# Kernel tuning notes

Hardware: AMD Instinct MI355X
Metric: run time of the kernel (lower is better)

## Reference

```python
import jax, jax.numpy as jnp
import numpy as np

B, T, C, H = 2, 2048, 512, 8
HD = C // H  # head size = 64

def _layernorm(x, g, b, eps=1e-5):
    mu = jnp.mean(x, axis=-1, keepdims=True)
    var = jnp.var(x, axis=-1, keepdims=True)
    return (x - mu) * jax.lax.rsqrt(var + eps) * g + b

def setup_inputs() -> dict:
    key = jax.random.key(0)
    ks = jax.random.split(key, 12)
    s_attn = 1.0 / np.sqrt(C)
    s_proj = 1.0 / np.sqrt(H * HD)
    s_ffn1 = 1.0 / np.sqrt(C)
    s_ffn2 = 1.0 / np.sqrt(4 * C)
    return {
        "x":   jax.random.normal(ks[0], (B, T, C), jnp.float32),
        "Wq":  jax.random.uniform(ks[1], (H, C, HD), jnp.float32, -s_attn, s_attn),
        "Wk":  jax.random.uniform(ks[2], (H, C, HD), jnp.float32, -s_attn, s_attn),
        "Wv":  jax.random.uniform(ks[3], (H, C, HD), jnp.float32, -s_attn, s_attn),
        "Wo":  jax.random.uniform(ks[4], (H * HD, C), jnp.float32, -s_proj, s_proj),
        "bo":  jax.random.uniform(ks[5], (C,), jnp.float32, -s_proj, s_proj),
        "W1":  jax.random.uniform(ks[6], (C, 4 * C), jnp.float32, -s_ffn1, s_ffn1),
        "b1":  jax.random.uniform(ks[7], (4 * C,), jnp.float32, -s_ffn1, s_ffn1),
        "W2":  jax.random.uniform(ks[8], (4 * C, C), jnp.float32, -s_ffn2, s_ffn2),
        "b2":  jax.random.uniform(ks[9], (C,), jnp.float32, -s_ffn2, s_ffn2),
        "g1":  jnp.ones((C,), jnp.float32),
        "be1": jnp.zeros((C,), jnp.float32),
        "g2":  jnp.ones((C,), jnp.float32),
        "be2": jnp.zeros((C,), jnp.float32),
    }

def reference(x, Wq, Wk, Wv, Wo, bo, W1, b1, W2, b2, g1, be1, g2, be2):
    # --- multi-head causal self-attention on ln1(x) ---
    h = _layernorm(x, g1, be1)
    q = jnp.einsum("btc,hcd->bhtd", h, Wq)
    k = jnp.einsum("btc,hcd->bhtd", h, Wk)
    v = jnp.einsum("btc,hcd->bhtd", h, Wv)
    scores = jnp.einsum("bhtd,bhsd->bhts", q, k) * (HD ** -0.5)
    causal = jnp.tril(jnp.ones((T, T), bool))
    scores = jnp.where(causal, scores, -jnp.inf)
    wei = jax.nn.softmax(scores, axis=-1)
    attn = jnp.einsum("bhts,bhsd->bhtd", wei, v)
    attn = attn.transpose(0, 2, 1, 3).reshape(B, T, H * HD)  # concat heads
    x = x + attn @ Wo + bo
    # --- GELU MLP on ln2(x) ---
    h2 = _layernorm(x, g2, be2)
    ff = jax.nn.gelu(h2 @ W1 + b1, approximate=False) @ W2 + b2
    return x + ff
```

## Files before the change

kernel.cpp:

```cpp
#include <hip/hip_runtime.h>
#include <math.h>

constexpr int B_   = 2;
constexpr int T_   = 2048;
constexpr int C_   = 512;
constexpr int H_   = 8;
constexpr int HD_  = 64;
constexpr int M_   = B_ * T_;
constexpr int FF_  = 4 * C_;
constexpr int NQKV_ = 3 * C_;

typedef __attribute__((ext_vector_type(8))) short short8;
typedef __attribute__((ext_vector_type(4))) short short4v;
typedef __attribute__((ext_vector_type(4))) float floatx4;

static __device__ __forceinline__ unsigned short f2bf(float f) {
    union { float f; unsigned u; } v; v.f = f;
    unsigned r = v.u + 0x7fff + ((v.u >> 16) & 1);
    return (unsigned short)(r >> 16);
}

static __device__ __forceinline__ unsigned packbf2(float a, float b) {
    union { float f; unsigned u; } x, y; x.f = a; y.f = b;
    unsigned lo = (x.u + 0x7fff + ((x.u >> 16) & 1)) >> 16;
    unsigned hi = (y.u + 0x7fff + ((y.u >> 16) & 1)) & 0xffff0000u;
    return lo | hi;
}

static __device__ __forceinline__ void gl2lds16(const unsigned short* g,
                                                unsigned short* l) {
    __builtin_amdgcn_global_load_lds(
        (const __attribute__((address_space(1))) void*)g,
        (__attribute__((address_space(3))) void*)l, 16, 0, 0);
}

#if __has_builtin(__builtin_amdgcn_mfma_f32_16x16x16bf16_1k)
static __device__ __forceinline__ floatx4 mfma16(short4v a, short4v b, floatx4 c) {
    return __builtin_amdgcn_mfma_f32_16x16x16bf16_1k(a, b, c, 0, 0, 0);
}
#elif __has_builtin(__builtin_amdgcn_mfma_f32_16x16x16_bf16)
static __device__ __forceinline__ floatx4 mfma16(short4v a, short4v b, floatx4 c) {
    return __builtin_amdgcn_mfma_f32_16x16x16_bf16(a, b, c, 0, 0, 0);
}
#else
static __device__ __forceinline__ floatx4 mfma16(short4v a, short4v b, floatx4 c) {
    asm volatile("v_mfma_f32_16x16x16_bf16 %0, %1, %2, %0"
                 : "+v"(c) : "v"(a), "v"(b));
    return c;
}
#endif

__global__ void prep_weights(const float* __restrict__ Wq,
                             const float* __restrict__ Wk,
                             const float* __restrict__ Wv,
                             const float* __restrict__ Wo,
                             const float* __restrict__ W1,
                             const float* __restrict__ W2,
                             unsigned short* __restrict__ Wqkv_t,
                             unsigned short* __restrict__ Wo_t,
                             unsigned short* __restrict__ W1_t,
                             unsigned short* __restrict__ W2_t) {
    __shared__ float tile[32][33];
    int idx = blockIdx.x;
    const float* src; unsigned short* dst;
    int K, N, k0, n0;
    float scale = 1.0f;
    if (idx < 768) {
        int wz = idx >> 8, rem = idx & 255;
        int h = rem >> 5, r2 = rem & 31;
        k0 = (r2 >> 1) * 32; n0 = (r2 & 1) * 32;
        src = (wz == 0 ? Wq : (wz == 1 ? Wk : Wv)) + (size_t)h * C_ * HD_;
        dst = Wqkv_t + (size_t)(wz * C_ + h * HD_) * C_;
        K = C_; N = HD_;
        if (wz == 0) scale = 0.125f;
    } else if (idx < 1024) {
        int rem = idx - 768;
        n0 = (rem & 15) * 32; k0 = (rem >> 4) * 32;
        src = Wo; dst = Wo_t; K = C_; N = C_;
    } else if (idx < 2048) {
        int rem = idx - 1024;
        n0 = (rem & 63) * 32; k0 = (rem >> 6) * 32;
        src = W1; dst = W1_t; K = C_; N = FF_;
    } else {
        int rem = idx - 2048;
        n0 = (rem & 15) * 32; k0 = (rem >> 4) * 32;
        src = W2; dst = W2_t; K = FF_; N = C_;
    }
    int tx = threadIdx.x, ty = threadIdx.y;
#pragma unroll
    for (int i = 0; i < 4; i++)
        tile[ty + i * 8][tx] = src[(size_t)(k0 + ty + i * 8) * N + n0 + tx];
    __syncthreads();
#pragma unroll
    for (int i = 0; i < 4; i++)
        dst[(size_t)(n0 + ty + i * 8) * K + k0 + tx] = f2bf(tile[tx][ty + i * 8] * scale);
}

__global__ void v_transpose(const unsigned short* __restrict__ qkv,
                            unsigned short* __restrict__ vT) {
    __shared__ unsigned short tile[32][33];
    int bh = blockIdx.z, b = bh >> 3, h = bh & 7;
    int t0 = blockIdx.x * 32, d0 = blockIdx.y * 32;
    int tx = threadIdx.x, ty = threadIdx.y;
#pragma unroll
    for (int i = 0; i < 4; i++)
        tile[ty + i * 8][tx] = qkv[(size_t)(b * T_ + t0 + ty + i * 8) * NQKV_
                                   + 2 * C_ + h * HD_ + d0 + tx];
    __syncthreads();
#pragma unroll
    for (int i = 0; i < 4; i++)
        vT[(size_t)(bh * HD_ + d0 + ty + i * 8) * T_ + t0 + tx] = tile[tx][ty + i * 8];
}

__global__ void ln_kernel(const float* __restrict__ x,
                          const float* __restrict__ g,
                          const float* __restrict__ b,
                          unsigned short* __restrict__ out) {
    int row  = blockIdx.x;
    int lane = threadIdx.x;
    const float* xr = x + (size_t)row * C_;
    int c0 = lane * 8;
    float4 v0 = *(const float4*)(xr + c0);
    float4 v1 = *(const float4*)(xr + c0 + 4);
    float vals[8] = {v0.x, v0.y, v0.z, v0.w, v1.x, v1.y, v1.z, v1.w};

    float s = 0.f, ss = 0.f;
#pragma unroll
    for (int j = 0; j < 8; j++) { s += vals[j]; ss += vals[j] * vals[j]; }
#pragma unroll
    for (int off = 32; off; off >>= 1) {
        s  += __shfl_xor(s,  off);
        ss += __shfl_xor(ss, off);
    }
    float mu  = s / C_;
    float var = ss / C_ - mu * mu;
    float rs  = rsqrtf(var + 1e-5f);

    unsigned short* orow = out + (size_t)row * C_;
#pragma unroll
    for (int j = 0; j < 8; j++) {
        int c = c0 + j;
        orow[c] = f2bf((vals[j] - mu) * rs * g[c] + b[c]);
    }
}

template<int BM, int BN, int BK>
__global__ __launch_bounds__(256) void mfma_gemm(
        const unsigned short* __restrict__ A,
        const unsigned short* __restrict__ Bt,
        const float* __restrict__ bias,
        const float* __restrict__ resid,
        float* __restrict__ outF,
        unsigned short* __restrict__ outB,
        int M, int N, int K, int flags) {
    constexpr int WM = BM / 2, WN = BN / 2;
    constexpr int MI = WM / 16, NI = WN / 16, KH = BK / 32;
    __shared__ unsigned short As[KH * BM * 32];
    __shared__ unsigned short Bs[KH * BN * 32];

    int t = threadIdx.x;
    int lane = t & 63, w = t >> 6;
    int wr = (w >> 1) * WM, wc = (w & 1) * WN;
    int lm = lane & 15, lq = lane >> 4;
    int m0 = blockIdx.y * BM, n0 = blockIdx.x * BN;

    floatx4 acc[MI][NI];
#pragma unroll
    for (int mi = 0; mi < MI; mi++)
#pragma unroll
        for (int ni = 0; ni < NI; ni++) acc[mi][ni] = (floatx4){0.f, 0.f, 0.f, 0.f};

    for (int k0 = 0; k0 < K; k0 += BK) {
        __syncthreads();
#pragma unroll
        for (int hh = 0; hh < KH; hh++) {
#pragma unroll
            for (int j = 0; j < BM * 4 / 256; j++) {
                int i = t + j * 256;
                gl2lds16(A + (size_t)(m0 + (i >> 2)) * K + k0 + hh * 32 + (i & 3) * 8,
                         &As[hh * BM * 32 + i * 8]);
            }
#pragma unroll
            for (int j = 0; j < BN * 4 / 256; j++) {
                int i = t + j * 256;
                gl2lds16(Bt + (size_t)(n0 + (i >> 2)) * K + k0 + hh * 32 + (i & 3) * 8,
                         &Bs[hh * BN * 32 + i * 8]);
            }
        }
        __syncthreads();

#pragma unroll
        for (int hh = 0; hh < KH; hh++) {
            short8 af[MI], bfv[NI];
#pragma unroll
            for (int mi = 0; mi < MI; mi++)
                af[mi] = *(const short8*)&As[hh * BM * 32 + (wr + mi * 16 + lm) * 32 + lq * 8];
#pragma unroll
            for (int ni = 0; ni < NI; ni++)
                bfv[ni] = *(const short8*)&Bs[hh * BN * 32 + (wc + ni * 16 + lm) * 32 + lq * 8];
#pragma unroll
            for (int mi = 0; mi < MI; mi++)
#pragma unroll
                for (int ni = 0; ni < NI; ni++)
                    acc[mi][ni] = __builtin_amdgcn_mfma_f32_16x16x32_bf16(
                        af[mi], bfv[ni], acc[mi][ni], 0, 0, 0);
        }
    }

#pragma unroll
    for (int mi = 0; mi < MI; mi++)
#pragma unroll
        for (int ni = 0; ni < NI; ni++) {
            int gc = n0 + wc + ni * 16 + lm;
#pragma unroll
            for (int r = 0; r < 4; r++) {
                int gr = m0 + wr + mi * 16 + lq * 4 + r;
                float v = acc[mi][ni][r];
                if (flags & 1) v += bias[gc];
                if (flags & 4) v = 0.5f * v * (1.0f + erff(v * 0.70710678118654752f));
                if (flags & 2) v += resid[(size_t)gr * N + gc];
                if (flags & 8) outB[(size_t)gr * N + gc] = f2bf(v);
                else           outF[(size_t)gr * N + gc] = v;
            }
        }
}

__global__ __launch_bounds__(256, 4) void attn_mfma(
        const unsigned short* __restrict__ qkv,
        const unsigned short* __restrict__ vT,
        float* __restrict__ oP,
        float* __restrict__ lP) {
    __shared__ unsigned short Ks[2][64 * 72];
    __shared__ unsigned short Vt[2][64 * 72];

    int t = threadIdx.x;
    int wq = t >> 6, lane = t & 63;
    int lm = lane & 15, quad = lane >> 4;
    int bh = blockIdx.y, b = bh >> 3, h = bh & 7;
    int tile = blockIdx.x >> 1, s = blockIdx.x & 1;
    int q0 = tile * 64;

    int srow = t >> 2, sq4 = t & 3;

    const unsigned short* kbase = qkv + (size_t)(b * T_) * NQKV_ + C_ + h * HD_;
    const unsigned short* vbase = vT + (size_t)(bh * HD_ + srow) * T_;

    int gq_row = q0 + wq * 16 + lm;
    const unsigned short* qp = qkv + (size_t)(b * T_ + gq_row) * NQKV_ + h * HD_;
    short8 qf0 = *(const short8*)(qp + quad * 8);
    short8 qf1 = *(const short8*)(qp + 32 + quad * 8);

    float l_s = 0.f;
    floatx4 o_acc[4];
#pragma unroll
    for (int dt = 0; dt < 4; dt++) o_acc[dt] = (floatx4){0.f, 0.f, 0.f, 0.f};

    short8 kp0, kp1, vp0, vp1;
    if (s <= tile) {
        int s0 = s * 64;
        const unsigned short* kg = kbase + (size_t)(s0 + srow) * NQKV_ + sq4 * 16;
        kp0 = *(const short8*)kg;
        kp1 = *(const short8*)(kg + 8);
        vp0 = *(const short8*)(vbase + s0 + sq4 * 16);
        vp1 = *(const short8*)(vbase + s0 + sq4 * 16 + 8);
        *(short8*)&Ks[0][srow * 72 + sq4 * 16]     = kp0;
        *(short8*)&Ks[0][srow * 72 + sq4 * 16 + 8] = kp1;
        *(short8*)&Vt[0][srow * 72 + sq4 * 16]     = vp0;
        *(short8*)&Vt[0][srow * 72 + sq4 * 16 + 8] = vp1;
    }

    int buf = 0;
    for (int c = s; c <= tile; c += 2) {
        bool havenext = (c + 2 <= tile);
        if (havenext) {
            int s0n = (c + 2) * 64;
            const unsigned short* kgn = kbase + (size_t)(s0n + srow) * NQKV_ + sq4 * 16;
            kp0 = *(const short8*)kgn;
            kp1 = *(const short8*)(kgn + 8);
            vp0 = *(const short8*)(vbase + s0n + sq4 * 16);
            vp1 = *(const short8*)(vbase + s0n + sq4 * 16 + 8);
        }
        __syncthreads();

        bool diag = (c == tile);
#pragma unroll
        for (int kt = 0; kt < 4; kt++) {
            if (diag && kt > wq) continue;
            short8 kf0 = *(const short8*)&Ks[buf][(kt * 16 + lm) * 72 + quad * 8];
            short8 kf1 = *(const short8*)&Ks[buf][(kt * 16 + lm) * 72 + 32 + quad * 8];
            floatx4 sv = (floatx4){0.f, 0.f, 0.f, 0.f};
            sv = __builtin_amdgcn_mfma_f32_16x16x32_bf16(kf0, qf0, sv, 0, 0, 0);
            sv = __builtin_amdgcn_mfma_f32_16x16x32_bf16(kf1, qf1, sv, 0, 0, 0);
            float p0, p1, p2, p3;
            {
                bool e = diag && (kt == wq);
                p0 = (e && (quad * 4 + 0 > lm)) ? 0.f : __expf(sv[0]);
                p1 = (e && (quad * 4 + 1 > lm)) ? 0.f : __expf(sv[1]);
                p2 = (e && (quad * 4 + 2 > lm)) ? 0.f : __expf(sv[2]);
                p3 = (e && (quad * 4 + 3 > lm)) ? 0.f : __expf(sv[3]);
            }
            l_s += (p0 + p1) + (p2 + p3);
            uint2 pu;
            pu.x = packbf2(p0, p1);
            pu.y = packbf2(p2, p3);
            short4v pk = *(short4v*)&pu;
#pragma unroll
            for (int dt = 0; dt < 4; dt++) {
                short4v vf = *(const short4v*)&Vt[buf][(dt * 16 + lm) * 72 + kt * 16 + quad * 4];
                o_acc[dt] = mfma16(pk, vf, o_acc[dt]);
            }
        }
        if (havenext) {
            int nb = buf ^ 1;
            *(short8*)&Ks[nb][srow * 72 + sq4 * 16]     = kp0;
            *(short8*)&Ks[nb][srow * 72 + sq4 * 16 + 8] = kp1;
            *(short8*)&Vt[nb][srow * 72 + sq4 * 16]     = vp0;
            *(short8*)&Vt[nb][srow * 72 + sq4 * 16 + 8] = vp1;
        }
        buf ^= 1;
    }

    float lsum = l_s;
    lsum += __shfl_xor(lsum, 16);
    lsum += __shfl_xor(lsum, 32);
    if (quad == 0)
        lP[(size_t)s * M_ * H_ + (size_t)(b * T_ + q0 + wq * 16 + lm) * H_ + h] = lsum;
    float* obase = oP + (size_t)s * M_ * C_;
#pragma unroll
    for (int r = 0; r < 4; r++) {
        int gq = q0 + wq * 16 + quad * 4 + r;
        float* op = obase + (size_t)(b * T_ + gq) * C_ + h * HD_ + lm;
#pragma unroll
        for (int dt = 0; dt < 4; dt++)
            op[dt * 16] = o_acc[dt][r];
    }
}

__global__ void attn_combine(const float* __restrict__ oP,
                             const float* __restrict__ lP,
                             unsigned short* __restrict__ o) {
    int row = blockIdx.x * 4 + (threadIdx.x >> 6);
    int lane = threadIdx.x & 63;
    int h = lane >> 3;
    float l0 = lP[(size_t)row * H_ + h];
    float l1 = lP[(size_t)M_ * H_ + (size_t)row * H_ + h];
    float inv = 1.f / (l0 + l1);
    int c0 = lane * 8;
    const float* p0 = oP + (size_t)row * C_ + c0;
    const float* p1 = oP + (size_t)M_ * C_ + (size_t)row * C_ + c0;
    unsigned short* op = o + (size_t)row * C_ + c0;
    float4 a0 = *(const float4*)p0;
    float4 a1 = *(const float4*)(p0 + 4);
    float4 b0 = *(const float4*)p1;
    float4 b1 = *(const float4*)(p1 + 4);
    op[0] = f2bf((a0.x + b0.x) * inv);
    op[1] = f2bf((a0.y + b0.y) * inv);
    op[2] = f2bf((a0.z + b0.z) * inv);
    op[3] = f2bf((a0.w + b0.w) * inv);
    op[4] = f2bf((a1.x + b1.x) * inv);
    op[5] = f2bf((a1.y + b1.y) * inv);
    op[6] = f2bf((a1.z + b1.z) * inv);
    op[7] = f2bf((a1.w + b1.w) * inv);
}

extern "C" void kernel_launch(void* const* d_in, const int* in_sizes, int n_in,
                              void* d_out, int out_size, void* d_ws, size_t ws_size,
                              hipStream_t stream) {
    const float* x   = (const float*)d_in[0];
    const float* Wq  = (const float*)d_in[1];
    const float* Wk  = (const float*)d_in[2];
    const float* Wv  = (const float*)d_in[3];
    const float* Wo  = (const float*)d_in[4];
    const float* bo  = (const float*)d_in[5];
    const float* W1  = (const float*)d_in[6];
    const float* b1  = (const float*)d_in[7];
    const float* W2  = (const float*)d_in[8];
    const float* b2  = (const float*)d_in[9];
    const float* g1  = (const float*)d_in[10];
    const float* be1 = (const float*)d_in[11];
    const float* g2  = (const float*)d_in[12];
    const float* be2 = (const float*)d_in[13];
    float* out = (float*)d_out;

    unsigned short* Wqkv_t = (unsigned short*)d_ws;
    unsigned short* Wo_t   = Wqkv_t + (size_t)NQKV_ * C_;
    unsigned short* W1_t   = Wo_t   + (size_t)C_ * C_;
    unsigned short* W2_t   = W1_t   + (size_t)C_ * FF_;
    unsigned short* hb     = W2_t   + (size_t)FF_ * C_;
    unsigned short* attnb  = hb     + (size_t)M_ * C_;
    unsigned short* qkvb   = attnb  + (size_t)M_ * C_;
    unsigned short* vTb    = qkvb   + (size_t)M_ * NQKV_;
    float*          oPf    = (float*)(vTb + (size_t)M_ * C_);
    float*          lPf    = oPf + 2 * (size_t)M_ * C_;
    unsigned short* ff1    = attnb;

    prep_weights<<<3072, dim3(32, 8), 0, stream>>>(
        Wq, Wk, Wv, Wo, W1, W2, Wqkv_t, Wo_t, W1_t, W2_t);

    ln_kernel<<<M_, 64, 0, stream>>>(x, g1, be1, hb);

    mfma_gemm<64, 128, 64><<<dim3(NQKV_ / 128, M_ / 64), 256, 0, stream>>>(
        hb, Wqkv_t, nullptr, nullptr, nullptr, qkvb, M_, NQKV_, C_, 8);

    v_transpose<<<dim3(T_ / 32, HD_ / 32, B_ * H_), dim3(32, 8), 0, stream>>>(
        qkvb, vTb);

    attn_mfma<<<dim3(64, B_ * H_), 256, 0, stream>>>(qkvb, vTb, oPf, lPf);

    attn_combine<<<M_ / 4, 256, 0, stream>>>(oPf, lPf, attnb);

    mfma_gemm<64, 64, 64><<<dim3(C_ / 64, M_ / 64), 256, 0, stream>>>(
        attnb, Wo_t, bo, x, out, nullptr, M_, C_, C_, 1 | 2);

    ln_kernel<<<M_, 64, 0, stream>>>(out, g2, be2, hb);

    mfma_gemm<64, 128, 64><<<dim3(FF_ / 128, M_ / 64), 256, 0, stream>>>(
        hb, W1_t, b1, nullptr, nullptr, ff1, M_, FF_, C_, 1 | 4 | 8);

    mfma_gemm<64, 64, 64><<<dim3(C_ / 64, M_ / 64), 256, 0, stream>>>(
        ff1, W2_t, b2, out, out, nullptr, M_, C_, FF_, 1 | 2);
}
```

Measured before the change: 225.1 us.

## Fuse V transpose into QKV GEMM, merge prologue kernels, store attention partials in bf16

Folds the first layernorm into the weight-prep kernel, writes V transposed straight from the QKV GEMM epilogue through LDS (dropping the separate v_transpose launch and its buffer pass), and packs LN blocks as four rows per 256-thread block. Attention split partial outputs are stored as bf16 instead of fp32, which halves the traffic into attn_combine. The aim is fewer launches and less memory traffic, at the cost of extra rounding on the partial sums and an LDS-staged epilogue in the GEMM.

```diff
diff --git a/kernel.cpp b/kernel.cpp
--- a/kernel.cpp
+++ b/kernel.cpp
@@ -20,6 +20,10 @@
     return (unsigned short)(r >> 16);
 }
 
+static __device__ __forceinline__ float bf2f(unsigned short s) {
+    union { unsigned u; float f; } v; v.u = (unsigned)s << 16; return v.f;
+}
+
 static __device__ __forceinline__ unsigned packbf2(float a, float b) {
     union { float f; unsigned u; } x, y; x.f = a; y.f = b;
     unsigned lo = (x.u + 0x7fff + ((x.u >> 16) & 1)) >> 16;
@@ -50,18 +54,54 @@
 }
 #endif
 
-__global__ void prep_weights(const float* __restrict__ Wq,
-                             const float* __restrict__ Wk,
-                             const float* __restrict__ Wv,
-                             const float* __restrict__ Wo,
-                             const float* __restrict__ W1,
-                             const float* __restrict__ W2,
-                             unsigned short* __restrict__ Wqkv_t,
-                             unsigned short* __restrict__ Wo_t,
-                             unsigned short* __restrict__ W1_t,
-                             unsigned short* __restrict__ W2_t) {
+static __device__ __forceinline__ void ln_row(int row, int lane,
+                                              const float* __restrict__ x,
+                                              const float* __restrict__ g,
+                                              const float* __restrict__ b,
+                                              unsigned short* __restrict__ out) {
+    const float* xr = x + (size_t)row * C_;
+    int c0 = lane * 8;
+    float4 v0 = *(const float4*)(xr + c0);
+    float4 v1 = *(const float4*)(xr + c0 + 4);
+    float vals[8] = {v0.x, v0.y, v0.z, v0.w, v1.x, v1.y, v1.z, v1.w};
+
+    float s = 0.f, ss = 0.f;
+#pragma unroll
+    for (int j = 0; j < 8; j++) { s += vals[j]; ss += vals[j] * vals[j]; }
+#pragma unroll
+    for (int off = 32; off; off >>= 1) {
+        s  += __shfl_xor(s,  off);
+        ss += __shfl_xor(ss, off);
+    }
+    float mu  = s / C_;
+    float var = ss / C_ - mu * mu;
+    float rs  = rsqrtf(var + 1e-5f);
+
+    unsigned short* orow = out + (size_t)row * C_;
+#pragma unroll
+    for (int j = 0; j < 8; j++) {
+        int c = c0 + j;
+        orow[c] = f2bf((vals[j] - mu) * rs * g[c] + b[c]);
+    }
+}
+
+__global__ __launch_bounds__(256) void prologue(
+        const float* __restrict__ Wq, const float* __restrict__ Wk,
+        const float* __restrict__ Wv, const float* __restrict__ Wo,
+        const float* __restrict__ W1, const float* __restrict__ W2,
+        const float* __restrict__ x,  const float* __restrict__ g1,
+        const float* __restrict__ be1,
+        unsigned short* __restrict__ Wqkv_t, unsigned short* __restrict__ Wo_t,
+        unsigned short* __restrict__ W1_t,   unsigned short* __restrict__ W2_t,
+        unsigned short* __restrict__ hb) {
+    int idx = blockIdx.x;
+    int tid = threadIdx.x;
+    if (idx >= 3072) {
+        int row = (idx - 3072) * 4 + (tid >> 6);
+        ln_row(row, tid & 63, x, g1, be1, hb);
+        return;
+    }
     __shared__ float tile[32][33];
-    int idx = blockIdx.x;
     const float* src; unsigned short* dst;
     int K, N, k0, n0;
     float scale = 1.0f;
@@ -86,7 +126,7 @@
         n0 = (rem & 15) * 32; k0 = (rem >> 4) * 32;
         src = W2; dst = W2_t; K = FF_; N = C_;
     }
-    int tx = threadIdx.x, ty = threadIdx.y;
+    int tx = tid & 31, ty = tid >> 5;
 #pragma unroll
     for (int i = 0; i < 4; i++)
         tile[ty + i * 8][tx] = src[(size_t)(k0 + ty + i * 8) * N + n0 + tx];
@@ -96,52 +136,12 @@
         dst[(size_t)(n0 + ty + i * 8) * K + k0 + tx] = f2bf(tile[tx][ty + i * 8] * scale);
 }
 
-__global__ void v_transpose(const unsigned short* __restrict__ qkv,
-                            unsigned short* __restrict__ vT) {
-    __shared__ unsigned short tile[32][33];
-    int bh = blockIdx.z, b = bh >> 3, h = bh & 7;
-    int t0 = blockIdx.x * 32, d0 = blockIdx.y * 32;
-    int tx = threadIdx.x, ty = threadIdx.y;
-#pragma unroll
-    for (int i = 0; i < 4; i++)
-        tile[ty + i * 8][tx] = qkv[(size_t)(b * T_ + t0 + ty + i * 8) * NQKV_
-                                   + 2 * C_ + h * HD_ + d0 + tx];
-    __syncthreads();
-#pragma unroll
-    for (int i = 0; i < 4; i++)
-        vT[(size_t)(bh * HD_ + d0 + ty + i * 8) * T_ + t0 + tx] = tile[tx][ty + i * 8];
-}
-
-__global__ void ln_kernel(const float* __restrict__ x,
-                          const float* __restrict__ g,
-                          const float* __restrict__ b,
-                          unsigned short* __restrict__ out) {
-    int row  = blockIdx.x;
-    int lane = threadIdx.x;
-    const float* xr = x + (size_t)row * C_;
-    int c0 = lane * 8;
-    float4 v0 = *(const float4*)(xr + c0);
-    float4 v1 = *(const float4*)(xr + c0 + 4);
-    float vals[8] = {v0.x, v0.y, v0.z, v0.w, v1.x, v1.y, v1.z, v1.w};
-
-    float s = 0.f, ss = 0.f;
-#pragma unroll
-    for (int j = 0; j < 8; j++) { s += vals[j]; ss += vals[j] * vals[j]; }
-#pragma unroll
-    for (int off = 32; off; off >>= 1) {
-        s  += __shfl_xor(s,  off);
-        ss += __shfl_xor(ss, off);
-    }
-    float mu  = s / C_;
-    float var = ss / C_ - mu * mu;
-    float rs  = rsqrtf(var + 1e-5f);
-
-    unsigned short* orow = out + (size_t)row * C_;
-#pragma unroll
-    for (int j = 0; j < 8; j++) {
-        int c = c0 + j;
-        orow[c] = f2bf((vals[j] - mu) * rs * g[c] + b[c]);
-    }
+__global__ __launch_bounds__(256) void ln_kernel(
+        const float* __restrict__ x, const float* __restrict__ g,
+        const float* __restrict__ b, unsigned short* __restrict__ out) {
+    int tid = threadIdx.x;
+    int row = blockIdx.x * 4 + (tid >> 6);
+    ln_row(row, tid & 63, x, g, b, out);
 }
 
 template<int BM, int BN, int BK>
@@ -152,11 +152,13 @@
         const float* __restrict__ resid,
         float* __restrict__ outF,
         unsigned short* __restrict__ outB,
+        unsigned short* __restrict__ vT,
         int M, int N, int K, int flags) {
     constexpr int WM = BM / 2, WN = BN / 2;
     constexpr int MI = WM / 16, NI = WN / 16, KH = BK / 32;
-    __shared__ unsigned short As[KH * BM * 32];
-    __shared__ unsigned short Bs[KH * BN * 32];
+    __shared__ unsigned short smem[KH * (BM + BN) * 32];
+    unsigned short* As = smem;
+    unsigned short* Bs = smem + KH * BM * 32;
 
     int t = threadIdx.x;
     int lane = t & 63, w = t >> 6;
@@ -205,6 +207,32 @@
                     acc[mi][ni] = __builtin_amdgcn_mfma_f32_16x16x32_bf16(
                         af[mi], bfv[ni], acc[mi][ni], 0, 0, 0);
         }
+    }
+
+    if ((flags & 16) && n0 >= 2 * C_) {
+        __syncthreads();
+        unsigned short* Ts = smem;
+#pragma unroll
+        for (int mi = 0; mi < MI; mi++)
+#pragma unroll
+            for (int ni = 0; ni < NI; ni++) {
+                int cl = wc + ni * 16 + lm;
+#pragma unroll
+                for (int r = 0; r < 4; r++)
+                    Ts[cl * 72 + wr + mi * 16 + lq * 4 + r] = f2bf(acc[mi][ni][r]);
+            }
+        __syncthreads();
+        int b = m0 >> 11, trow = m0 & (T_ - 1);
+#pragma unroll
+        for (int it = 0; it < BN * (BM / 8) / 256; it++) {
+            int u = it * 256 + t;
+            int cl = u >> 3, seg = u & 7;
+            int vcol = n0 - 2 * C_ + cl;
+            int hh2 = vcol >> 6, dd = vcol & 63;
+            short8 vv = *(const short8*)&Ts[cl * 72 + seg * 8];
+            *(short8*)&vT[(size_t)((b * H_ + hh2) * HD_ + dd) * T_ + trow + seg * 8] = vv;
+        }
+        return;
     }
 
 #pragma unroll
@@ -228,7 +256,7 @@
 __global__ __launch_bounds__(256, 4) void attn_mfma(
         const unsigned short* __restrict__ qkv,
         const unsigned short* __restrict__ vT,
-        float* __restrict__ oP,
+        unsigned short* __restrict__ oP,
         float* __restrict__ lP) {
     __shared__ unsigned short Ks[2][64 * 72];
     __shared__ unsigned short Vt[2][64 * 72];
@@ -325,20 +353,21 @@
     lsum += __shfl_xor(lsum, 32);
     if (quad == 0)
         lP[(size_t)s * M_ * H_ + (size_t)(b * T_ + q0 + wq * 16 + lm) * H_ + h] = lsum;
-    float* obase = oP + (size_t)s * M_ * C_;
+    unsigned short* obase = oP + (size_t)s * M_ * C_;
 #pragma unroll
     for (int r = 0; r < 4; r++) {
         int gq = q0 + wq * 16 + quad * 4 + r;
-        float* op = obase + (size_t)(b * T_ + gq) * C_ + h * HD_ + lm;
+        unsigned short* op = obase + (size_t)(b * T_ + gq) * C_ + h * HD_ + lm;
 #pragma unroll
         for (int dt = 0; dt < 4; dt++)
-            op[dt * 16] = o_acc[dt][r];
-    }
-}
-
-__global__ void attn_combine(const float* __restrict__ oP,
-                             const float* __restrict__ lP,
-                             unsigned short* __restrict__ o) {
+            op[dt * 16] = f2bf(o_acc[dt][r]);
+    }
+}
+
+__global__ __launch_bounds__(256) void attn_combine(
+        const unsigned short* __restrict__ oP,
+        const float* __restrict__ lP,
+        unsigned short* __restrict__ o) {
     int row = blockIdx.x * 4 + (threadIdx.x >> 6);
     int lane = threadIdx.x & 63;
     int h = lane >> 3;
@@ -346,21 +375,14 @@
     float l1 = lP[(size_t)M_ * H_ + (size_t)row * H_ + h];
     float inv = 1.f / (l0 + l1);
     int c0 = lane * 8;
-    const float* p0 = oP + (size_t)row * C_ + c0;
-    const float* p1 = oP + (size_t)M_ * C_ + (size_t)row * C_ + c0;
+    const unsigned short* p0 = oP + (size_t)row * C_ + c0;
+    const unsigned short* p1 = oP + (size_t)M_ * C_ + (size_t)row * C_ + c0;
     unsigned short* op = o + (size_t)row * C_ + c0;
-    float4 a0 = *(const float4*)p0;
-    float4 a1 = *(const float4*)(p0 + 4);
-    float4 b0 = *(const float4*)p1;
-    float4 b1 = *(const float4*)(p1 + 4);
-    op[0] = f2bf((a0.x + b0.x) * inv);
-    op[1] = f2bf((a0.y + b0.y) * inv);
-    op[2] = f2bf((a0.z + b0.z) * inv);
-    op[3] = f2bf((a0.w + b0.w) * inv);
-    op[4] = f2bf((a1.x + b1.x) * inv);
-    op[5] = f2bf((a1.y + b1.y) * inv);
-    op[6] = f2bf((a1.z + b1.z) * inv);
-    op[7] = f2bf((a1.w + b1.w) * inv);
+    short8 a = *(const short8*)p0;
+    short8 b = *(const short8*)p1;
+#pragma unroll
+    for (int j = 0; j < 8; j++)
+        op[j] = f2bf((bf2f((unsigned short)a[j]) + bf2f((unsigned short)b[j])) * inv);
 }
 
 extern "C" void kernel_launch(void* const* d_in, const int* in_sizes, int n_in,
@@ -390,33 +412,28 @@
     unsigned short* attnb  = hb     + (size_t)M_ * C_;
     unsigned short* qkvb   = attnb  + (size_t)M_ * C_;
     unsigned short* vTb    = qkvb   + (size_t)M_ * NQKV_;
-    float*          oPf    = (float*)(vTb + (size_t)M_ * C_);
-    float*          lPf    = oPf + 2 * (size_t)M_ * C_;
+    unsigned short* oPb    = vTb    + (size_t)M_ * C_;
+    float*          lPf    = (float*)(oPb + 2 * (size_t)M_ * C_);
     unsigned short* ff1    = attnb;
 
-    prep_weights<<<3072, dim3(32, 8), 0, stream>>>(
-        Wq, Wk, Wv, Wo, W1, W2, Wqkv_t, Wo_t, W1_t, W2_t);
-
-    ln_kernel<<<M_, 64, 0, stream>>>(x, g1, be1, hb);
+    prologue<<<4096, 256, 0, stream>>>(Wq, Wk, Wv, Wo, W1, W2, x, g1, be1,
+                                       Wqkv_t, Wo_t, W1_t, W2_t, hb);
 
     mfma_gemm<64, 128, 64><<<dim3(NQKV_ / 128, M_ / 64), 256, 0, stream>>>(
-        hb, Wqkv_t, nullptr, nullptr, nullptr, qkvb, M_, NQKV_, C_, 8);
-
-    v_transpose<<<dim3(T_ / 32, HD_ / 32, B_ * H_), dim3(32, 8), 0, stream>>>(
-        qkvb, vTb);
-
-    attn_mfma<<<dim3(64, B_ * H_), 256, 0, stream>>>(qkvb, vTb, oPf, lPf);
-
-    attn_combine<<<M_ / 4, 256, 0, stream>>>(oPf, lPf, attnb);
+        hb, Wqkv_t, nullptr, nullptr, nullptr, qkvb, vTb, M_, NQKV_, C_, 8 | 16);
+
+    attn_mfma<<<dim3(64, B_ * H_), 256, 0, stream>>>(qkvb, vTb, oPb, lPf);
+
+    attn_combine<<<M_ / 4, 256, 0, stream>>>(oPb, lPf, attnb);
 
     mfma_gemm<64, 64, 64><<<dim3(C_ / 64, M_ / 64), 256, 0, stream>>>(
-        attnb, Wo_t, bo, x, out, nullptr, M_, C_, C_, 1 | 2);
-
-    ln_kernel<<<M_, 64, 0, stream>>>(out, g2, be2, hb);
+        attnb, Wo_t, bo, x, out, nullptr, nullptr, M_, C_, C_, 1 | 2);
+
+    ln_kernel<<<M_ / 4, 256, 0, stream>>>(out, g2, be2, hb);
 
     mfma_gemm<64, 128, 64><<<dim3(FF_ / 128, M_ / 64), 256, 0, stream>>>(
-        hb, W1_t, b1, nullptr, nullptr, ff1, M_, FF_, C_, 1 | 4 | 8);
+        hb, W1_t, b1, nullptr, nullptr, ff1, nullptr, M_, FF_, C_, 1 | 4 | 8);
 
     mfma_gemm<64, 64, 64><<<dim3(C_ / 64, M_ / 64), 256, 0, stream>>>(
-        ff1, W2_t, b2, out, out, nullptr, M_, C_, FF_, 1 | 2);
-}
+        ff1, W2_t, b2, out, out, nullptr, nullptr, M_, C_, FF_, 1 | 2);
+}
```

After: 219.2 us. 2.6% less time.
